# Kernel optimization log

Hardware: AMD Instinct MI355X
Metric: run time of the kernel (lower is better)

The kernel has to match this reference:

```python
import jax, jax.numpy as jnp
import numpy as np

BS, NR, VDIM, QDIM, CSUB, RDIM = 64, 36, 2048, 1024, 512, 256


def setup_inputs() -> dict:
    key = jax.random.key(0)
    ks = jax.random.split(key, 8)
    s = 0.02  # weight scale
    return {
        "X": jax.random.normal(ks[0], (BS, NR, VDIM), jnp.float32),
        "Q": jax.random.normal(ks[1], (BS, QDIM), jnp.float32),
        "pos": jax.random.uniform(ks[2], (BS, NR, 4), jnp.float32),
        "Wv": jax.random.normal(ks[3], (VDIM + 4, CSUB), jnp.float32) * s,
        "bv": jnp.zeros((CSUB,), jnp.float32),
        "Wq": jax.random.normal(ks[4], (QDIM, CSUB), jnp.float32) * s,
        "bq": jnp.zeros((CSUB,), jnp.float32),
        "W1": jax.random.normal(ks[5], (CSUB, RDIM), jnp.float32) * s,
        "b1": jnp.zeros((RDIM,), jnp.float32),
        "W2": jax.random.normal(ks[6], (RDIM, RDIM), jnp.float32) * s,
        "b2": jnp.zeros((RDIM,), jnp.float32),
    }


def reference(X, Q, pos, Wv, bv, Wq, bq, W1, b1, W2, b2):
    # pe_enable: concat position encodings -> [bs, Nr, v_dim+4]
    Xc = jnp.concatenate([X, pos], axis=-1)
    # FCNet projections (weight-norm linear + ReLU; dropout identity in eval)
    Xp = jax.nn.relu(Xc @ Wv + bv)              # [bs, Nr, C]
    Qp = jax.nn.relu(Q @ Wq + bq)               # [bs, C]
    Xs = Xp + Qp[:, None, :]                    # broadcast question over regions
    # pairwise elementwise product: pair[b,i,j,c] = Xs[b,j,c] * Xs[b,i,c]
    pair = Xs[:, None, :, :] * Xs[:, :, None, :]  # [bs, Nr, Nr, C]
    # 1x1 convs == per-(i,j) channel-mixing matmuls, relu (dropout identity)
    h = jax.nn.relu(jnp.einsum('bijc,cr->bijr', pair, W1) + b1)
    r_emb = jax.nn.relu(jnp.einsum('bijr,rs->bijs', h, W2) + b2)
    return r_emb  # [bs, Nr, Nr, r_dim]
```

## Files before the change

kernel.cpp:

```cpp
#include <hip/hip_runtime.h>
#include <hip/hip_bf16.h>
#include <stdint.h>

#define BSZ 64
#define NRG 36
#define VD  2048
#define QD  1024
#define CS  512
#define RD  256
#define KP  2080
#define MR  (BSZ*NRG)
#define TRI  666
#define TRIQ 768

typedef __bf16 bf16x8 __attribute__((ext_vector_type(8)));
typedef float  f32x4  __attribute__((ext_vector_type(4)));

static __device__ __forceinline__ f32x4 mfma16(bf16x8 a, bf16x8 b, f32x4 c) {
    return __builtin_amdgcn_mfma_f32_16x16x32_bf16(a, b, c, 0, 0, 0);
}

static __device__ __forceinline__ void load_lds16(const __bf16* g, __bf16* l) {
    __builtin_amdgcn_global_load_lds(
        (const __attribute__((address_space(1))) uint32_t*)(const void*)g,
        (__attribute__((address_space(3))) uint32_t*)(void*)l,
        16, 0, 0);
}

__global__ __launch_bounds__(256) void k_prep(
    const float* __restrict__ X, const float* __restrict__ pos,
    const float* __restrict__ Wv, const float* __restrict__ W1,
    const float* __restrict__ W2,
    const float* __restrict__ Q, const float* __restrict__ Wq,
    const float* __restrict__ bq,
    __bf16* __restrict__ Xc, __bf16* __restrict__ Wvg,
    __bf16* __restrict__ W1g, __bf16* __restrict__ W2g,
    int* __restrict__ lut, float* __restrict__ Qp)
{
    int id = blockIdx.x;
    if (id < MR) {
        const float* xr = X + (size_t)id * VD;
        const float* pr = pos + (size_t)id * 4;
        __bf16* o = Xc + (size_t)id * KP;
        for (int c = threadIdx.x; c < KP; c += 256) {
            float v = 0.f;
            if (c < VD) v = xr[c];
            else if (c < VD + 4) v = pr[c - VD];
            o[c] = (__bf16)v;
        }
        return;
    }
    id -= MR;
    if (id < 520 + 64 + 32) {
        const float* W; __bf16* Wg; int K, N, nbx;
        if (id < 520)      {          W = Wv; Wg = Wvg; K = VD + 4; N = CS; nbx = CS / 64; }
        else if (id < 584) { id -= 520; W = W1; Wg = W1g; K = CS;     N = RD; nbx = RD / 64; }
        else               { id -= 584; W = W2; Wg = W2g; K = RD;     N = RD; nbx = RD / 64; }
        int bx = id % nbx, by = id / nbx;
        int g = by * 4 + (threadIdx.x >> 6);
        int n = bx * 64 + (threadIdx.x & 63);
        bf16x8 v;
        #pragma unroll
        for (int e = 0; e < 8; ++e) {
            int k = g * 8 + e;
            v[e] = (__bf16)((k < K) ? W[(size_t)k * N + n] : 0.f);
        }
        *(bf16x8*)(Wg + ((size_t)g * N + n) * 8) = v;
        return;
    }
    id -= 616;
    if (id == 0) {
        for (int t = threadIdx.x; t < TRIQ; t += 256) {
            int tt = (t < TRI) ? t : (TRI - 1);
            int i = 0;
            while (tt >= NRG - i) { tt -= NRG - i; ++i; }
            lut[t] = (i << 8) | (i + tt);
        }
        return;
    }
    id -= 1;
    {
        int b   = id >> 3;
        int col = (id & 7) * 64 + (threadIdx.x & 63);
        int ks  = threadIdx.x >> 6;
        const float* q = Q  + (size_t)b * QD + ks * 256;
        const float* w = Wq + (size_t)(ks * 256) * CS + col;
        float acc = 0.f;
        #pragma unroll 8
        for (int k = 0; k < 256; ++k)
            acc = fmaf(q[k], w[(size_t)k * CS], acc);
        __shared__ float red[256];
        red[threadIdx.x] = acc;
        __syncthreads();
        if (ks == 0) {
            float v = red[threadIdx.x] + red[threadIdx.x + 64]
                    + red[threadIdx.x + 128] + red[threadIdx.x + 192] + bq[col];
            Qp[(size_t)b * CS + col] = fmaxf(v, 0.f);
        }
    }
}

__global__ __launch_bounds__(256) void k_g1(
    const __bf16* __restrict__ Xc,
    const __bf16* __restrict__ Wvg,
    const float* __restrict__ bv,
    const float* __restrict__ Qp,
    __bf16* __restrict__ Xs)
{
    __shared__ __align__(16) __bf16 sA[4][4 * 64 * 8];
    __shared__ __align__(16) __bf16 sB[4][4 * 64 * 8];

    const int tid = threadIdx.x;
    const int lane = tid & 63;
    const int w = tid >> 6;
    const int wm = w & 1, wn = w >> 1;
    const int l15 = lane & 15, l4 = lane >> 4;
    const int m0 = blockIdx.x * 64;
    const int n0 = blockIdx.y * 64;
    const int sg = tid >> 6;
    const int sr = tid & 63;

    auto stage = [&](int kt, int slot) {
        load_lds16(Xc + (size_t)(m0 + sr) * KP + kt * 32 + sg * 8,
                   &sA[slot][0] + (size_t)tid * 8);
        load_lds16(Wvg + ((size_t)(kt * 4 + sg) * CS + n0 + sr) * 8,
                   &sB[slot][0] + (size_t)tid * 8);
    };

    constexpr int NKT = KP / 32;
    stage(0, 0);
    stage(1, 1);

    f32x4 acc[2][2] = {};
    for (int kt = 0; kt < NKT; ++kt) {
        if (kt + 2 < NKT) stage(kt + 2, (kt + 2) & 3);
        if (kt + 2 < NKT)      asm volatile("s_waitcnt vmcnt(4)" ::: "memory");
        else if (kt + 1 < NKT) asm volatile("s_waitcnt vmcnt(2)" ::: "memory");
        else                   asm volatile("s_waitcnt vmcnt(0)" ::: "memory");
        __builtin_amdgcn_s_barrier();

        const __bf16* a_base = &sA[kt & 3][0];
        const __bf16* b_base = &sB[kt & 3][0];
        bf16x8 af[2], bf[2];
        #pragma unroll
        for (int f = 0; f < 2; ++f)
            af[f] = *(const bf16x8*)(a_base + ((size_t)l4 * 64 + wm * 32 + f * 16 + l15) * 8);
        #pragma unroll
        for (int g = 0; g < 2; ++g)
            bf[g] = *(const bf16x8*)(b_base + ((size_t)l4 * 64 + wn * 32 + g * 16 + l15) * 8);
        __builtin_amdgcn_s_setprio(1);
        #pragma unroll
        for (int f = 0; f < 2; ++f)
            #pragma unroll
            for (int g = 0; g < 2; ++g)
                acc[f][g] = mfma16(af[f], bf[g], acc[f][g]);
        __builtin_amdgcn_s_setprio(0);
    }

    #pragma unroll
    for (int f = 0; f < 2; ++f) {
        int row0 = m0 + wm * 32 + f * 16 + l4 * 4;
        #pragma unroll
        for (int g = 0; g < 2; ++g) {
            int col = n0 + wn * 32 + g * 16 + l15;
            float bb = bv[col];
            #pragma unroll
            for (int r = 0; r < 4; ++r) {
                int row = row0 + r;
                float v = fmaxf(acc[f][g][r] + bb, 0.f) + Qp[(size_t)(row / NRG) * CS + col];
                Xs[(size_t)row * CS + col] = (__bf16)v;
            }
        }
    }
}

__global__ __launch_bounds__(768, 1) void k_g23(
    const __bf16* __restrict__ Xs,
    const __bf16* __restrict__ W1g,
    const __bf16* __restrict__ W2g,
    const float* __restrict__ b1,
    const float* __restrict__ b2,
    float* __restrict__ Out,
    const int* __restrict__ lut)
{
    __shared__ __align__(16) __bf16 uni[32 * 192 * 8];
    __shared__ __align__(16) __bf16 sW[2][4 * RD * 8];

    const int tid = threadIdx.x;
    const int lane = tid & 63;
    const int w = tid >> 6;
    const int mg = w >> 1;
    const int nh = w & 1;
    const int l15 = lane & 15, l4 = lane >> 4;
    const int b = blockIdx.y;
    const int r_base = blockIdx.x * 192;
    const char* sXc = (const char*)uni;

    {
        const __bf16* src = Xs + (size_t)b * NRG * CS;
        #pragma unroll
        for (int it = 0; it < 3; ++it) {
            int id = it * 768 + tid;
            int r = id >> 6, cp = id & 63;
            bf16x8 v = *(const bf16x8*)(src + (size_t)r * CS + cp * 8);
            int ba = (r << 10) | ((cp ^ (r & 7)) << 4);
            *(bf16x8*)((char*)uni + ba) = v;
        }
    }
    const int t0 = r_base + mg * 32 + l15;
    const int ij0 = lut[t0], ij1 = lut[t0 + 16];
    const int i0 = ij0 >> 8, j0 = ij0 & 255;
    const int i1 = ij1 >> 8, j1 = ij1 & 255;

    asm volatile("s_waitcnt lgkmcnt(0)" ::: "memory");
    __builtin_amdgcn_s_barrier();

    const bool stager = (tid < 256);
#define STG(SRC, KT, SLOT) { \
    _Pragma("unroll") for (int it_ = 0; it_ < 4; ++it_) { \
        int c_ = tid + it_ * 256; \
        load_lds16((SRC) + (size_t)(KT) * (RD * 32) + (size_t)c_ * 8, \
                   &sW[SLOT][0] + (size_t)c_ * 8); } }

    if (stager) STG(W1g, 0, 0)

    f32x4 acc[2][8] = {};
    for (int kt = 0; kt < 16; ++kt) {
        if (stager) asm volatile("s_waitcnt vmcnt(0)" ::: "memory");
        __builtin_amdgcn_s_barrier();
        if (stager) {
            if (kt < 15) { STG(W1g, kt + 1, (kt + 1) & 1) }
            else         { STG(W2g, 0, 0) }
        }
        const int kc = kt * 4 + l4;
        bf16x8 xi0 = *(const bf16x8*)(sXc + ((i0 << 10) | ((kc ^ (i0 & 7)) << 4)));
        bf16x8 xj0 = *(const bf16x8*)(sXc + ((j0 << 10) | ((kc ^ (j0 & 7)) << 4)));
        bf16x8 xi1 = *(const bf16x8*)(sXc + ((i1 << 10) | ((kc ^ (i1 & 7)) << 4)));
        bf16x8 xj1 = *(const bf16x8*)(sXc + ((j1 << 10) | ((kc ^ (j1 & 7)) << 4)));
        bf16x8 af0, af1;
        #pragma unroll
        for (int e = 0; e < 8; ++e) {
            af0[e] = (__bf16)((float)xi0[e] * (float)xj0[e]);
            af1[e] = (__bf16)((float)xi1[e] * (float)xj1[e]);
        }
        const __bf16* wb = &sW[kt & 1][0];
        __builtin_amdgcn_s_setprio(1);
        #pragma unroll
        for (int g = 0; g < 8; ++g) {
            bf16x8 wf = *(const bf16x8*)(wb + ((size_t)l4 * RD + nh * 128 + g * 16 + l15) * 8);
            acc[0][g] = mfma16(af0, wf, acc[0][g]);
            acc[1][g] = mfma16(af1, wf, acc[1][g]);
        }
        __builtin_amdgcn_s_setprio(0);
    }

    __builtin_amdgcn_s_barrier();

    #pragma unroll
    for (int g = 0; g < 8; ++g) {
        int col = nh * 128 + g * 16 + l15;
        float bb = b1[col];
        int kc2 = col >> 3, e = col & 7;
        #pragma unroll
        for (int fm = 0; fm < 2; ++fm) {
            int row0 = mg * 32 + fm * 16 + l4 * 4;
            #pragma unroll
            for (int r = 0; r < 4; ++r) {
                float v = fmaxf(acc[fm][g][r] + bb, 0.f);
                uni[((size_t)kc2 * 192 + row0 + r) * 8 + e] = (__bf16)v;
            }
        }
    }
    asm volatile("s_waitcnt lgkmcnt(0)" ::: "memory");
    __builtin_amdgcn_s_barrier();

    f32x4 acc2[2][8] = {};
    for (int kt = 0; kt < 8; ++kt) {
        if (stager) asm volatile("s_waitcnt vmcnt(0)" ::: "memory");
        __builtin_amdgcn_s_barrier();
        if (stager && kt < 7) STG(W2g, kt + 1, (kt + 1) & 1)
        bf16x8 ah0, ah1;
        {
            int row0 = mg * 32 + l15;
            ah0 = *(const bf16x8*)(uni + ((size_t)(kt * 4 + l4) * 192 + row0) * 8);
            ah1 = *(const bf16x8*)(uni + ((size_t)(kt * 4 + l4) * 192 + row0 + 16) * 8);
        }
        const __bf16* wb = &sW[kt & 1][0];
        __builtin_amdgcn_s_setprio(1);
        #pragma unroll
        for (int g = 0; g < 8; ++g) {
            bf16x8 wf = *(const bf16x8*)(wb + ((size_t)l4 * RD + nh * 128 + g * 16 + l15) * 8);
            acc2[0][g] = mfma16(ah0, wf, acc2[0][g]);
            acc2[1][g] = mfma16(ah1, wf, acc2[1][g]);
        }
        __builtin_amdgcn_s_setprio(0);
    }

    float bias2[8];
    #pragma unroll
    for (int g = 0; g < 8; ++g) bias2[g] = b2[nh * 128 + g * 16 + l15];
    #pragma unroll
    for (int fm = 0; fm < 2; ++fm) {
        int rw = mg * 32 + fm * 16 + l4 * 4;
        #pragma unroll
        for (int r = 0; r < 4; ++r) {
            int t = r_base + rw + r;
            if (t < TRI) {
                int ij = lut[t];
                int i = ij >> 8, j = ij & 255;
                float* o1 = Out + ((size_t)((b * NRG + i) * NRG + j)) * RD;
                float* o2 = Out + ((size_t)((b * NRG + j) * NRG + i)) * RD;
                #pragma unroll
                for (int g = 0; g < 8; ++g) {
                    int col = nh * 128 + g * 16 + l15;
                    float v = fmaxf(acc2[fm][g][r] + bias2[g], 0.f);
                    o1[col] = v; o2[col] = v;
                }
            }
        }
    }
#undef STG
}

extern "C" void kernel_launch(void* const* d_in, const int* in_sizes, int n_in,
                              void* d_out, int out_size, void* d_ws, size_t ws_size,
                              hipStream_t stream) {
    const float* X   = (const float*)d_in[0];
    const float* Q   = (const float*)d_in[1];
    const float* pos = (const float*)d_in[2];
    const float* Wv  = (const float*)d_in[3];
    const float* bv  = (const float*)d_in[4];
    const float* Wq  = (const float*)d_in[5];
    const float* bq  = (const float*)d_in[6];
    const float* W1  = (const float*)d_in[7];
    const float* b1  = (const float*)d_in[8];
    const float* W2  = (const float*)d_in[9];
    const float* b2  = (const float*)d_in[10];

    char* ws = (char*)d_ws;
    size_t off = 0;
    auto alloc = [&](size_t bytes) {
        char* p = ws + off;
        off = (off + bytes + 255) & ~(size_t)255;
        return p;
    };
    __bf16* Xc  = (__bf16*)alloc((size_t)MR * KP * 2);
    __bf16* Wvg = (__bf16*)alloc((size_t)(KP/8) * CS * 8 * 2);
    __bf16* W1g = (__bf16*)alloc((size_t)(CS/8) * RD * 8 * 2);
    __bf16* W2g = (__bf16*)alloc((size_t)(RD/8) * RD * 8 * 2);
    float*  Qp  = (float*) alloc((size_t)BSZ * CS * 4);
    __bf16* Xs  = (__bf16*)alloc((size_t)MR * CS * 2);
    int*    lut = (int*)   alloc((size_t)TRIQ * 4);

    hipLaunchKernelGGL(k_prep, dim3(MR + 616 + 1 + 512), dim3(256), 0, stream,
                       X, pos, Wv, W1, W2, Q, Wq, bq,
                       Xc, Wvg, W1g, W2g, lut, Qp);
    hipLaunchKernelGGL(k_g1, dim3(MR/64, CS/64), dim3(256), 0, stream,
                       Xc, Wvg, bv, Qp, Xs);
    hipLaunchKernelGGL(k_g23, dim3(4, BSZ), dim3(768), 0, stream,
                       Xs, W1g, W2g, b1, b2, (float*)d_out, (const int*)lut);
}
```

Baseline: 98.82 us.

## Deepen weight staging to four LDS slots with two-ahead prefetch in fused MLP

The fused pairwise MLP kernel now keeps four LDS weight buffers instead of two. It issues weight tile loads two iterations ahead and waits with partial vmcnt counts rather than draining every load before each step, so global-to-LDS latency can overlap more compute across both GEMM phases. Separately, the Qp projection loop now splits its dot product across four independent accumulators to shorten the FMA dependency chain. The change costs more LDS per block, and correctness depends on the vmcnt accounting and on slot reuse with a single barrier per iteration.

```diff
diff --git a/kernel.cpp b/kernel.cpp
--- a/kernel.cpp
+++ b/kernel.cpp
@@ -85,12 +85,16 @@
         int ks  = threadIdx.x >> 6;
         const float* q = Q  + (size_t)b * QD + ks * 256;
         const float* w = Wq + (size_t)(ks * 256) * CS + col;
-        float acc = 0.f;
-        #pragma unroll 8
-        for (int k = 0; k < 256; ++k)
-            acc = fmaf(q[k], w[(size_t)k * CS], acc);
+        float a0 = 0.f, a1 = 0.f, a2 = 0.f, a3 = 0.f;
+        #pragma unroll 4
+        for (int k = 0; k < 256; k += 4) {
+            a0 = fmaf(q[k],     w[(size_t)(k)     * CS], a0);
+            a1 = fmaf(q[k + 1], w[(size_t)(k + 1) * CS], a1);
+            a2 = fmaf(q[k + 2], w[(size_t)(k + 2) * CS], a2);
+            a3 = fmaf(q[k + 3], w[(size_t)(k + 3) * CS], a3);
+        }
         __shared__ float red[256];
-        red[threadIdx.x] = acc;
+        red[threadIdx.x] = a0 + a1 + a2 + a3;
         __syncthreads();
         if (ks == 0) {
             float v = red[threadIdx.x] + red[threadIdx.x + 64]
@@ -184,7 +188,7 @@
     const int* __restrict__ lut)
 {
     __shared__ __align__(16) __bf16 uni[32 * 192 * 8];
-    __shared__ __align__(16) __bf16 sW[2][4 * RD * 8];
+    __shared__ __align__(16) __bf16 sW[4][4 * RD * 8];
 
     const int tid = threadIdx.x;
     const int lane = tid & 63;
@@ -215,24 +219,28 @@
     asm volatile("s_waitcnt lgkmcnt(0)" ::: "memory");
     __builtin_amdgcn_s_barrier();
 
-    const bool stager = (tid < 256);
-#define STG(SRC, KT, SLOT) { \
-    _Pragma("unroll") for (int it_ = 0; it_ < 4; ++it_) { \
-        int c_ = tid + it_ * 256; \
-        load_lds16((SRC) + (size_t)(KT) * (RD * 32) + (size_t)c_ * 8, \
-                   &sW[SLOT][0] + (size_t)c_ * 8); } }
-
-    if (stager) STG(W1g, 0, 0)
+    auto stg_t = [&](int t) {
+        if (tid < 256) {
+            const __bf16* src = (t < 16) ? (W1g + (size_t)t * (RD * 32))
+                                         : (W2g + (size_t)(t - 16) * (RD * 32));
+            __bf16* dst = &sW[t & 3][0];
+            #pragma unroll
+            for (int it = 0; it < 4; ++it) {
+                int c = tid + it * 256;
+                load_lds16(src + (size_t)c * 8, dst + (size_t)c * 8);
+            }
+        }
+    };
+
+    stg_t(0);
+    stg_t(1);
 
     f32x4 acc[2][8] = {};
-    for (int kt = 0; kt < 16; ++kt) {
-        if (stager) asm volatile("s_waitcnt vmcnt(0)" ::: "memory");
+    for (int t = 0; t < 16; ++t) {
+        stg_t(t + 2);
+        asm volatile("s_waitcnt vmcnt(8)" ::: "memory");
         __builtin_amdgcn_s_barrier();
-        if (stager) {
-            if (kt < 15) { STG(W1g, kt + 1, (kt + 1) & 1) }
-            else         { STG(W2g, 0, 0) }
-        }
-        const int kc = kt * 4 + l4;
+        const int kc = t * 4 + l4;
         bf16x8 xi0 = *(const bf16x8*)(sXc + ((i0 << 10) | ((kc ^ (i0 & 7)) << 4)));
         bf16x8 xj0 = *(const bf16x8*)(sXc + ((j0 << 10) | ((kc ^ (j0 & 7)) << 4)));
         bf16x8 xi1 = *(const bf16x8*)(sXc + ((i1 << 10) | ((kc ^ (i1 & 7)) << 4)));
@@ -243,7 +251,7 @@
             af0[e] = (__bf16)((float)xi0[e] * (float)xj0[e]);
             af1[e] = (__bf16)((float)xi1[e] * (float)xj1[e]);
         }
-        const __bf16* wb = &sW[kt & 1][0];
+        const __bf16* wb = &sW[t & 3][0];
         __builtin_amdgcn_s_setprio(1);
         #pragma unroll
         for (int g = 0; g < 8; ++g) {
@@ -275,17 +283,20 @@
     __builtin_amdgcn_s_barrier();
 
     f32x4 acc2[2][8] = {};
-    for (int kt = 0; kt < 8; ++kt) {
-        if (stager) asm volatile("s_waitcnt vmcnt(0)" ::: "memory");
+    for (int t = 16; t < 24; ++t) {
+        if (t + 2 < 24) stg_t(t + 2);
+        if (t + 2 < 24)      asm volatile("s_waitcnt vmcnt(8)" ::: "memory");
+        else if (t + 1 < 24) asm volatile("s_waitcnt vmcnt(4)" ::: "memory");
+        else                 asm volatile("s_waitcnt vmcnt(0)" ::: "memory");
         __builtin_amdgcn_s_barrier();
-        if (stager && kt < 7) STG(W2g, kt + 1, (kt + 1) & 1)
+        const int kt = t - 16;
         bf16x8 ah0, ah1;
         {
             int row0 = mg * 32 + l15;
             ah0 = *(const bf16x8*)(uni + ((size_t)(kt * 4 + l4) * 192 + row0) * 8);
             ah1 = *(const bf16x8*)(uni + ((size_t)(kt * 4 + l4) * 192 + row0 + 16) * 8);
         }
-        const __bf16* wb = &sW[kt & 1][0];
+        const __bf16* wb = &sW[t & 3][0];
         __builtin_amdgcn_s_setprio(1);
         #pragma unroll
         for (int g = 0; g < 8; ++g) {
@@ -319,7 +330,6 @@
             }
         }
     }
-#undef STG
 }
 
 extern "C" void kernel_launch(void* const* d_in, const int* in_sizes, int n_in,
```

Result: no change. 99.07 us (+0.3%).
